# Kernel tuning notes

Measured on AMD Instinct MI355X. Metric: run time of the kernel, lower is better.

Reference implementation:

```python
import jax, jax.numpy as jnp
import numpy as np

B, N1, N2, C = 4, 1024, 128, 1152
H, D = 16, 72            # num_heads, head_dim (1152 = 16*72)
HID = 4608               # mlp hidden = 4*1152
ATTN_SCALE = D ** -0.5
RMS_SCALE = C ** 0.5     # quirk: RMSNorm built with dim=1152 though applied over d=72
LN_EPS = 1e-6


def setup_inputs() -> dict:
    key = jax.random.key(0)
    ks = iter(jax.random.split(key, 64))
    n = lambda shape, s=1.0: jax.random.normal(next(ks), shape, jnp.float32) * s
    W = 0.02  # weight init scale
    inp = {
        "x": n((B, N1, C)),
        "c": n((B, N2, C)),
        "global_c": n((B, C)),
        "ada_x_w": n((C, 6 * C), W), "ada_x_b": jnp.zeros((6 * C,)),
        "ada_c_w": n((C, 6 * C), W), "ada_c_b": jnp.zeros((6 * C,)),
        "g1x_g": jnp.ones((C,)), "g1x_b": jnp.zeros((C,)),
        "g2x_g": jnp.ones((C,)), "g2x_b": jnp.zeros((C,)),
        "g1c_g": jnp.ones((C,)), "g1c_b": jnp.zeros((C,)),
        "g2c_g": jnp.ones((C,)), "g2c_b": jnp.zeros((C,)),
        "qkv_x_w": n((C, 3 * C), W), "qkv_x_b": jnp.zeros((3 * C,)),
        "proj_x_w": n((C, C), W), "proj_x_b": jnp.zeros((C,)),
        "qkv_c_w": n((C, 3 * C), W), "qkv_c_b": jnp.zeros((3 * C,)),
        "proj_c_w": n((C, C), W), "proj_c_b": jnp.zeros((C,)),
        "gq_x": jnp.ones((1,)), "gk_x": jnp.ones((1,)),
        "gq_c": jnp.ones((1,)), "gk_c": jnp.ones((1,)),
        "mlp_x_w1": n((C, HID), W), "mlp_x_b1": jnp.zeros((HID,)),
        "mlp_x_w2": n((HID, C), W), "mlp_x_b2": jnp.zeros((C,)),
        "mlp_c_w1": n((C, HID), W), "mlp_c_b1": jnp.zeros((HID,)),
        "mlp_c_w2": n((HID, C), W), "mlp_c_b2": jnp.zeros((C,)),
    }
    return inp


def _ln(t, g, b):
    m = t.mean(-1, keepdims=True)
    v = ((t - m) ** 2).mean(-1, keepdims=True)
    return (t - m) * jax.lax.rsqrt(v + LN_EPS) * g + b


def _modulate(t, shift, scale):  # shift/scale: [B, C]
    return t * (1.0 + scale[:, None, :]) + shift[:, None, :]


def _rms(t, g):  # F.normalize over last dim, then * sqrt(1152) * g
    nrm = jnp.sqrt(jnp.sum(t * t, axis=-1, keepdims=True))
    return t / jnp.maximum(nrm, 1e-12) * (RMS_SCALE * g)


def _heads(t):  # [B, N, H*D] -> [B, H, N, D]
    Bq, Nq, _ = t.shape
    return t.reshape(Bq, Nq, H, D).transpose(0, 2, 1, 3)


def _mmdit_forward(x, c, global_c,
                   ada_x_w, ada_x_b, ada_c_w, ada_c_b,
                   g1x_g, g1x_b, g2x_g, g2x_b, g1c_g, g1c_b, g2c_g, g2c_b,
                   qkv_x_w, qkv_x_b, proj_x_w, proj_x_b,
                   qkv_c_w, qkv_c_b, proj_c_w, proj_c_b,
                   gq_x, gk_x, gq_c, gk_c,
                   mlp_x_w1, mlp_x_b1, mlp_x_w2, mlp_x_b2,
                   mlp_c_w1, mlp_c_b1, mlp_c_w2, mlp_c_b2):
    s = jax.nn.silu(global_c)
    mod_x = jnp.split(s @ ada_x_w + ada_x_b, 6, axis=-1)
    mod_c = jnp.split(s @ ada_c_w + ada_c_b, 6, axis=-1)
    (sh_msa_x, sc_msa_x, gt_msa_x, sh_mlp_x, sc_mlp_x, gt_mlp_x) = mod_x
    (sh_msa_c, sc_msa_c, gt_msa_c, sh_mlp_c, sc_mlp_c, gt_mlp_c) = mod_c

    xin = _modulate(_ln(x, g1x_g, g1x_b), sh_msa_x, sc_msa_x)
    cin = _modulate(_ln(c, g1c_g, g1c_b), sh_msa_c, sc_msa_c)

    qx, kx, vx = jnp.split(xin @ qkv_x_w + qkv_x_b, 3, axis=-1)
    qc, kc, vc = jnp.split(cin @ qkv_c_w + qkv_c_b, 3, axis=-1)
    qx, kx, vx = _heads(qx), _heads(kx), _heads(vx)
    qc, kc, vc = _heads(qc), _heads(kc), _heads(vc)
    qx, kx = _rms(qx, gq_x), _rms(kx, gk_x)
    qc, kc = _rms(qc, gq_c), _rms(kc, gk_c)

    q = jnp.concatenate([qx, qc], axis=2)  # [B,H,N1+N2,D]
    k = jnp.concatenate([kx, kc], axis=2)
    v = jnp.concatenate([vx, vc], axis=2)

    scores = jnp.einsum('bhnd,bhmd->bhnm', q, k) * ATTN_SCALE
    attn = jax.nn.softmax(scores, axis=-1)
    o = jnp.einsum('bhnm,bhmd->bhnd', attn, v)
    o = o.transpose(0, 2, 1, 3).reshape(B, N1 + N2, C)
    ox, oc = o[:, :N1], o[:, N1:]
    attn_x = ox @ proj_x_w + proj_x_b
    attn_c = oc @ proj_c_w + proj_c_b

    x = x + gt_msa_x[:, None, :] * attn_x
    c = c + gt_msa_c[:, None, :] * attn_c

    hx = _modulate(_ln(x, g2x_g, g2x_b), sh_mlp_x, sc_mlp_x)
    hx = jax.nn.gelu(hx @ mlp_x_w1 + mlp_x_b1, approximate=True) @ mlp_x_w2 + mlp_x_b2
    x = x + gt_mlp_x[:, None, :] * hx

    hc = _modulate(_ln(c, g2c_g, g2c_b), sh_mlp_c, sc_mlp_c)
    hc = jax.nn.gelu(hc @ mlp_c_w1 + mlp_c_b1, approximate=True) @ mlp_c_w2 + mlp_c_b2
    c = c + gt_mlp_c[:, None, :] * hc
    return x, c


def reference(x, c, global_c,
              ada_x_w, ada_x_b, ada_c_w, ada_c_b,
              g1x_g, g1x_b, g2x_g, g2x_b, g1c_g, g1c_b, g2c_g, g2c_b,
              qkv_x_w, qkv_x_b, proj_x_w, proj_x_b,
              qkv_c_w, qkv_c_b, proj_c_w, proj_c_b,
              gq_x, gk_x, gq_c, gk_c,
              mlp_x_w1, mlp_x_b1, mlp_x_w2, mlp_x_b2,
              mlp_c_w1, mlp_c_b1, mlp_c_w2, mlp_c_b2):
    return _mmdit_forward(x, c, global_c,
                          ada_x_w, ada_x_b, ada_c_w, ada_c_b,
                          g1x_g, g1x_b, g2x_g, g2x_b, g1c_g, g1c_b, g2c_g, g2c_b,
                          qkv_x_w, qkv_x_b, proj_x_w, proj_x_b,
                          qkv_c_w, qkv_c_b, proj_c_w, proj_c_b,
                          gq_x, gk_x, gq_c, gk_c,
                          mlp_x_w1, mlp_x_b1, mlp_x_w2, mlp_x_b2,
                          mlp_c_w1, mlp_c_b1, mlp_c_w2, mlp_c_b2)
```

## Files before the change

### kernel.cpp

```cpp
#include <hip/hip_runtime.h>

typedef unsigned short u16;
typedef unsigned int u32;
typedef __attribute__((ext_vector_type(8))) short bf16x8;
typedef __attribute__((ext_vector_type(4))) float f32x4;

#define MX_ 4096
#define NT_ 1152
#define C_  1152
#define DP_ 96
#define D_  72
#define H_  16
#define MT_ 4608

static __device__ __forceinline__ float b2f(u16 u){ union{u32 i; float f;} x; x.i=((u32)u)<<16; return x.f; }
static __device__ __forceinline__ u16 f2b(float f){ u32 i=__float_as_uint(f); return (u16)((i + 0x7FFFu + ((i>>16)&1u))>>16); }

static __device__ __forceinline__ void gl_lds16(const u16* g, u16* l){
  __builtin_amdgcn_global_load_lds((const __attribute__((address_space(1))) void*)g,
                                   (__attribute__((address_space(3))) void*)l, 16, 0, 0);
}

#define MFMA16(a,b,c) __builtin_amdgcn_mfma_f32_16x16x32_bf16(a,b,c,0,0,0)

struct TrArgs {
  const float* src[8]; u16* dst[8]; int K[8]; int N[8]; int start[9];
};

__global__ __launch_bounds__(256) void transpose_kernel(TrArgs a){
  int bx = blockIdx.x;
  int mi = 0;
  #pragma unroll
  for (int i = 0; i < 8; ++i) if (bx >= a.start[i+1]) mi = i+1;
  int t = bx - a.start[mi];
  int K = a.K[mi], N = a.N[mi];
  int ntk = K >> 5;
  int tk = t % ntk, tn = t / ntk;
  int k0 = tk*32, n0 = tn*32;
  __shared__ u16 lds[32][33];
  int c = threadIdx.x & 31, r = threadIdx.x >> 5;
  const float* src = a.src[mi];
  u16* dst = a.dst[mi];
  #pragma unroll
  for (int ii = 0; ii < 4; ++ii){
    int row = r + ii*8;
    lds[row][c] = f2b(src[(size_t)(k0+row)*N + n0 + c]);
  }
  __syncthreads();
  {
    int n = threadIdx.x >> 3, kg = threadIdx.x & 7;
    union { uint2 v; u16 e[4]; } o;
    #pragma unroll
    for (int j = 0; j < 4; ++j) o.e[j] = lds[kg*4 + j][n];
    *(uint2*)(dst + (size_t)(n0+n)*K + k0 + kg*4) = o.v;
  }
}

__global__ __launch_bounds__(256) void ada_kernel(const float* gc, const float* wx, const float* bx,
                                                  const float* wc, const float* bc,
                                                  float* mod_x, float* mod_c){
  __shared__ float s[4][C_];
  __shared__ float part[4][4][64];
  int tid = threadIdx.x;
  for (int i = tid; i < 4*C_; i += 256){
    float v = gc[i];
    s[i / C_][i % C_] = v / (1.f + __expf(-v));
  }
  __syncthreads();
  int jq = tid & 63;
  int kq = tid >> 6;
  int jg = blockIdx.x*64 + jq;
  int which = jg / 6912;
  int j = jg % 6912;
  const float* W = which ? wc : wx;
  float a0=0.f, a1=0.f, a2=0.f, a3=0.f;
  for (int k = kq*288; k < kq*288 + 288; ++k){
    float w = W[(size_t)k*6912 + j];
    a0 += s[0][k]*w; a1 += s[1][k]*w; a2 += s[2][k]*w; a3 += s[3][k]*w;
  }
  part[kq][0][jq]=a0; part[kq][1][jq]=a1; part[kq][2][jq]=a2; part[kq][3][jq]=a3;
  __syncthreads();
  if (kq == 0){
    float bb = (which ? bc : bx)[j];
    float* out = which ? mod_c : mod_x;
    #pragma unroll
    for (int b = 0; b < 4; ++b){
      out[(size_t)b*6912 + j] = part[0][b][jq] + part[1][b][jq] + part[2][b][jq] + part[3][b][jq] + bb;
    }
  }
}

__global__ __launch_bounds__(256) void ln_mod_kernel(
  const float* srcx, const float* srcc, const float* g, const float* bt,
  const float* gcn, const float* btc,
  const float* shx, const float* scx, const float* shc, const float* scc,
  u16* out)
{
  int m = blockIdx.x;
  bool isC = (m >= MX_);
  const float* src = isC ? srcc + (size_t)(m - MX_)*C_ : srcx + (size_t)m*C_;
  int bidx = isC ? ((m - MX_) >> 7) : (m >> 10);
  const float* gg = isC ? gcn : g;
  const float* bb = isC ? btc : bt;
  const float* sh = (isC ? shc : shx) + (size_t)bidx*6912;
  const float* sc = (isC ? scc : scx) + (size_t)bidx*6912;
  int tid = threadIdx.x;
  float lv[8];
  float sum = 0.f, sq = 0.f;
  if (tid < 144){
    float4 v0 = *(const float4*)(src + tid*8);
    float4 v1 = *(const float4*)(src + tid*8 + 4);
    lv[0]=v0.x; lv[1]=v0.y; lv[2]=v0.z; lv[3]=v0.w;
    lv[4]=v1.x; lv[5]=v1.y; lv[6]=v1.z; lv[7]=v1.w;
    #pragma unroll
    for (int j = 0; j < 8; ++j){ sum += lv[j]; sq += lv[j]*lv[j]; }
  }
  #pragma unroll
  for (int off = 1; off < 64; off <<= 1){ sum += __shfl_xor(sum, off); sq += __shfl_xor(sq, off); }
  __shared__ float rs[4], rq[4];
  int wave = tid >> 6, lane = tid & 63;
  if (lane == 0){ rs[wave] = sum; rq[wave] = sq; }
  __syncthreads();
  float S = rs[0]+rs[1]+rs[2]+rs[3];
  float Q = rq[0]+rq[1]+rq[2]+rq[3];
  float mean = S * (1.f/1152.f);
  float var  = Q * (1.f/1152.f) - mean*mean;
  float rstd = rsqrtf(var + 1e-6f);
  if (tid < 144){
    union { uint4 v; u16 s[8]; } o;
    #pragma unroll
    for (int j = 0; j < 8; ++j){
      int n = tid*8 + j;
      float val = (lv[j] - mean)*rstd*gg[n] + bb[n];
      val = val*(1.f + sc[n]) + sh[n];
      o.s[j] = f2b(val);
    }
    *(uint4*)(out + (size_t)m*C_ + tid*8) = o.v;
  }
}

__global__ __launch_bounds__(256) void reduce2_kernel(
  const float* p0, const float* p1,
  const float* residx, const float* residc,
  const float* modx, const float* modc,
  const float* biasx, const float* biasc,
  float* outx, float* outc)
{
  for (int i4 = blockIdx.x*256 + threadIdx.x; i4 < MT_*288; i4 += gridDim.x*256){
    int m = i4 / 288, n4 = (i4 % 288)*4;
    bool isC = (m >= MX_);
    int bidx = isC ? ((m - MX_) >> 7) : (m >> 10);
    const float* gate  = (isC ? modc : modx) + (size_t)bidx*6912;
    const float* bias  = isC ? biasc : biasx;
    const float* resid = isC ? residc + (size_t)(m - MX_)*C_ : residx + (size_t)m*C_;
    float* o = isC ? outc + (size_t)(m - MX_)*C_ : outx + (size_t)m*C_;
    float4 a = *(const float4*)(p0 + (size_t)m*C_ + n4);
    float4 b = *(const float4*)(p1 + (size_t)m*C_ + n4);
    float4 r = *(const float4*)(resid + n4);
    float4 ov;
    ov.x = r.x + gate[n4+0]*(a.x + b.x + bias[n4+0]);
    ov.y = r.y + gate[n4+1]*(a.y + b.y + bias[n4+1]);
    ov.z = r.z + gate[n4+2]*(a.z + b.z + bias[n4+2]);
    ov.w = r.w + gate[n4+3]*(a.w + b.w + bias[n4+3]);
    *(float4*)(o + n4) = ov;
  }
}

struct GemmArgs {
  const u16* A; int lda; int rowmap;
  const u16* BTx; const u16* BTc;
  const float* biasx; const float* biasc;
  void* outx; void* outc;
  const float* residx; const float* residc;
  const float* gatex; const float* gatec;
  int N, K, kLen;
};

static __device__ __forceinline__ int amap(int m, int rowmap){
  if (rowmap){
    if (m < MX_) return (m >> 10)*NT_ + (m & 1023);
    int mm = m - MX_;
    return (mm >> 7)*NT_ + 1024 + (mm & 127);
  }
  return m;
}

template<int EPI>
__global__ __launch_bounds__(256, 2) void gemm_kernel(GemmArgs g){
  __shared__ u16 As[128*64];
  __shared__ u16 Bs[128*64];
  int gx = gridDim.x, gy = gridDim.y;
  int nwg = gx*gy;
  int orig = blockIdx.y*gx + blockIdx.x;
  int q = nwg >> 3, r8 = nwg & 7;
  int xcd = orig & 7, wi = orig >> 3;
  int swz = (xcd < r8 ? xcd*(q+1) : r8*(q+1) + (xcd - r8)*q) + wi;
  int n0 = (swz % gx)*128, m0 = (swz / gx)*128;
  int kStart = blockIdx.z * g.kLen;
  bool isC = (m0 >= MX_);
  const u16* BT = isC ? g.BTc : g.BTx;
  int tid = threadIdx.x, wave = tid >> 6, lane = tid & 63;
  int lg = lane >> 4, lr = lane & 15;
  int wm = wave >> 1, wn = wave & 1;
  f32x4 acc[4][4] = {};

  const u16* Aaddr[4]; const u16* Baddr[4];
  #pragma unroll
  for (int i = 0; i < 4; ++i){
    int cb = (wave*4 + i)*64;
    int qq = cb + lane;
    int row = qq >> 3;
    int c16 = (qq & 7) ^ (row & 7);
    Aaddr[i] = g.A + (size_t)amap(m0 + row, g.rowmap)*g.lda + kStart + c16*8;
    Baddr[i] = BT + (size_t)(n0 + row)*g.K + kStart + c16*8;
  }
  for (int k0 = 0; k0 < g.kLen; k0 += 64){
    #pragma unroll
    for (int i = 0; i < 4; ++i){
      int cb = (wave*4 + i)*64;
      gl_lds16(Aaddr[i] + k0, As + cb*8);
      gl_lds16(Baddr[i] + k0, Bs + cb*8);
    }
    __syncthreads();
    #pragma unroll
    for (int kkI = 0; kkI < 2; ++kkI){
      bf16x8 af[4], bfr[4];
      #pragma unroll
      for (int mi = 0; mi < 4; ++mi){
        int row = wm*64 + mi*16 + lr;
        int c16 = (kkI*4 + lg) ^ (row & 7);
        af[mi] = *(const bf16x8*)&As[row*64 + c16*8];
      }
      #pragma unroll
      for (int ni = 0; ni < 4; ++ni){
        int row = wn*64 + ni*16 + lr;
        int c16 = (kkI*4 + lg) ^ (row & 7);
        bfr[ni] = *(const bf16x8*)&Bs[row*64 + c16*8];
      }
      #pragma unroll
      for (int mi = 0; mi < 4; ++mi)
        #pragma unroll
        for (int ni = 0; ni < 4; ++ni)
          acc[mi][ni] = MFMA16(af[mi], bfr[ni], acc[mi][ni]);
    }
    __syncthreads();
  }

  const float* bias  = isC ? g.biasc : g.biasx;
  const float* resid = isC ? g.residc : g.residx;
  void* out = isC ? g.outc : g.outx;
  const float* gate = nullptr;
  if (EPI == 2){
    int bidx = isC ? ((m0 - MX_) >> 7) : (m0 >> 10);
    gate = (isC ? g.gatec : g.gatex) + (size_t)bidx*6912;
  }
  int mbase = isC ? (m0 - MX_) : m0;
  float* pbase = nullptr;
  if (EPI == 3) pbase = blockIdx.z ? (float*)g.outc : (float*)g.outx;
  #pragma unroll
  for (int mi = 0; mi < 4; ++mi){
    #pragma unroll
    for (int r = 0; r < 4; ++r){
      #pragma unroll
      for (int ni = 0; ni < 4; ++ni){
        int n = n0 + wn*64 + ni*16 + lr;
        if (EPI == 3){
          size_t prow = (size_t)(m0 + wm*64 + mi*16 + lg*4 + r);
          pbase[prow*(size_t)g.N + n] = acc[mi][ni][r];
        } else {
          size_t orow = (size_t)(mbase + wm*64 + mi*16 + lg*4 + r);
          float v = acc[mi][ni][r] + bias[n];
          if (EPI == 1){
            float u = 0.7978845608028654f*(v + 0.044715f*v*v*v);
            v = 0.5f*v*(1.f + tanhf(u));
          }
          if (EPI == 2){
            v = resid[orow*(size_t)g.N + n] + gate[n]*v;
            ((float*)out)[orow*(size_t)g.N + n] = v;
          } else {
            ((u16*)out)[orow*(size_t)g.N + n] = f2b(v);
          }
        }
      }
    }
  }
}

__global__ __launch_bounds__(256) void rmshead_kernel(
  const u16* qkv, const float* gqx, const float* gkx, const float* gqc, const float* gkc,
  u16* qpad, u16* kpad, u16* vT)
{
  int tt = blockIdx.x, h = blockIdx.y, b = blockIdx.z;
  int t0 = tt*64;
  bool isC = (t0 >= 1024);
  size_t rowbase = isC ? (size_t)(MX_ + b*128 + (t0 - 1024)) : (size_t)(b*1024 + t0);
  __shared__ u16 sq[2][64][72];
  __shared__ u16 sv[64][72];
  __shared__ float nf[2][64];
  int tid = threadIdx.x;
  for (int s = tid; s < 1728; s += 256){
    int which = s / 576, rem = s % 576;
    int t = rem / 9, ch = rem % 9;
    uint4 v = *(const uint4*)(qkv + (rowbase + t)*3456 + which*C_ + h*D_ + ch*8);
    u16* dst = (which < 2) ? &sq[which][t][ch*8] : &sv[t][ch*8];
    *(uint4*)dst = v;
  }
  __syncthreads();
  {
    int row = tid >> 1, half = tid & 1;
    int which = row >> 6, t = row & 63;
    float ss = 0.f;
    for (int d = half*36; d < half*36 + 36; ++d){
      float v = b2f(sq[which][t][d]); ss += v*v;
    }
    ss += __shfl_xor(ss, 1);
    if (half == 0){
      const float* gp = (which == 0) ? (isC ? gqc : gqx) : (isC ? gkc : gkx);
      float f = 33.9411254970f * gp[0] / fmaxf(sqrtf(ss), 1e-12f);
      if (which == 0) f *= 0.17002324581205f;
      nf[which][t] = f;
    }
  }
  __syncthreads();
  size_t obase = ((size_t)(b*H_ + h)*NT_ + t0) * DP_;
  for (int s = tid; s < 1536; s += 256){
    int which = s / 768, rem = s % 768;
    int t = rem / 12, ch = rem % 12;
    float f = nf[which][t];
    union { uint4 v; u16 e[8]; } o;
    #pragma unroll
    for (int j = 0; j < 8; ++j){
      int d = ch*8 + j;
      o.e[j] = (d < D_) ? f2b(b2f(sq[which][t][d]) * f) : (u16)0;
    }
    *(uint4*)((which == 0 ? qpad : kpad) + obase + (size_t)t*DP_ + ch*8) = o.v;
  }
  size_t vbase = (size_t)(b*H_ + h)*80*NT_;
  for (int s = tid; s < 576; s += 256){
    int d = s / 8, ch = s % 8;
    union { uint4 v; u16 e[8]; } o;
    #pragma unroll
    for (int j = 0; j < 8; ++j) o.e[j] = sv[ch*8 + j][d];
    *(uint4*)(vT + vbase + (size_t)d*NT_ + t0 + ch*8) = o.v;
  }
  for (int s = tid; s < 512; s += 256){
    int d = 72 + (s >> 6), t = s & 63;
    vT[vbase + (size_t)d*NT_ + t0 + t] = (d == 72) ? (u16)0x3F80 : (u16)0;
  }
}

__global__ __launch_bounds__(256) __attribute__((amdgpu_waves_per_eu(1, 2))) void attn_kernel(
  const u16* qpad, const u16* kpad, const u16* vT, u16* O)
{
  __shared__ u16 Ps[4][32][40];
  int orig = blockIdx.x;
  int w = (orig & 7)*72 + (orig >> 3);
  int qtb = w % 9, hb = w / 9;
  int h = hb & 15, b = hb >> 4;
  int bh = b*H_ + h;
  int tid = threadIdx.x, wave = tid >> 6, lane = tid & 63;
  int lg = lane >> 4, lr = lane & 15;
  int q0 = qtb*128 + wave*32;

  const u16* qb = qpad + (size_t)bh*NT_*DP_;
  const u16* kb = kpad + (size_t)bh*NT_*DP_;
  const u16* vb = vT + (size_t)bh*80*NT_;

  bf16x8 qf[2][3];
  #pragma unroll
  for (int qt = 0; qt < 2; ++qt)
    #pragma unroll
    for (int kk = 0; kk < 3; ++kk)
      qf[qt][kk] = *(const bf16x8*)(qb + (size_t)(q0 + qt*16 + lr)*DP_ + kk*32 + lg*8);

  f32x4 acc[5][2] = {};
  float m0 = -1e30f, m1 = -1e30f;

  bf16x8 kfA[2][3], kfB[2][3], vf[5];
  auto LOADK = [&](bf16x8 (&kf)[2][3], int kvt){
    #pragma unroll
    for (int kt = 0; kt < 2; ++kt)
      #pragma unroll
      for (int kk = 0; kk < 3; ++kk)
        kf[kt][kk] = *(const bf16x8*)(kb + (size_t)(kvt*32 + kt*16 + lr)*DP_ + kk*32 + lg*8);
  };
  u16* prow0 = &Ps[wave][lr][0];
  u16* prow1 = &Ps[wave][16 + lr][0];

  auto TILE = [&](bf16x8 (&kf)[2][3], bf16x8 (&kfn)[2][3], int t){
    #pragma unroll
    for (int dc = 0; dc < 5; ++dc)
      vf[dc] = *(const bf16x8*)(vb + (size_t)(dc*16 + lr)*NT_ + t*32 + lg*8);
    if (t + 1 < 36) LOADK(kfn, t + 1);

    f32x4 st[2][2] = {};
    __builtin_amdgcn_s_setprio(1);
    #pragma unroll
    for (int kk = 0; kk < 3; ++kk){
      st[0][0] = MFMA16(kf[0][kk], qf[0][kk], st[0][0]);
      st[0][1] = MFMA16(kf[0][kk], qf[1][kk], st[0][1]);
      st[1][0] = MFMA16(kf[1][kk], qf[0][kk], st[1][0]);
      st[1][1] = MFMA16(kf[1][kk], qf[1][kk], st[1][1]);
    }
    __builtin_amdgcn_s_setprio(0);

    float pm0 = fmaxf(fmaxf(fmaxf(st[0][0][0], st[0][0][1]), fmaxf(st[0][0][2], st[0][0][3])),
                      fmaxf(fmaxf(st[1][0][0], st[1][0][1]), fmaxf(st[1][0][2], st[1][0][3])));
    float pm1 = fmaxf(fmaxf(fmaxf(st[0][1][0], st[0][1][1]), fmaxf(st[0][1][2], st[0][1][3])),
                      fmaxf(fmaxf(st[1][1][0], st[1][1][1]), fmaxf(st[1][1][2], st[1][1][3])));
    float tt = fmaxf(pm0 - m0, pm1 - m1);
    if (!__all(tt <= 11.5415603f)){
      float r0 = fmaxf(pm0, __shfl_xor(pm0, 16)); r0 = fmaxf(r0, __shfl_xor(r0, 32));
      float r1 = fmaxf(pm1, __shfl_xor(pm1, 16)); r1 = fmaxf(r1, __shfl_xor(r1, 32));
      float n0 = fmaxf(m0, r0), n1 = fmaxf(m1, r1);
      float f0 = exp2f(m0 - n0), f1 = exp2f(m1 - n1);
      m0 = n0; m1 = n1;
      #pragma unroll
      for (int dc = 0; dc < 5; ++dc)
        #pragma unroll
        for (int j = 0; j < 4; ++j){ acc[dc][0][j] *= f0; acc[dc][1][j] *= f1; }
    }
    #pragma unroll
    for (int kt = 0; kt < 2; ++kt){
      #pragma unroll
      for (int qt = 0; qt < 2; ++qt){
        float mm = qt ? m1 : m0;
        float e0 = exp2f(st[kt][qt][0] - mm);
        float e1 = exp2f(st[kt][qt][1] - mm);
        float e2 = exp2f(st[kt][qt][2] - mm);
        float e3 = exp2f(st[kt][qt][3] - mm);
        u32 lo, hi;
        asm("v_cvt_pk_bf16_f32 %0, %1, %2" : "=v"(lo) : "v"(e0), "v"(e1));
        asm("v_cvt_pk_bf16_f32 %0, %1, %2" : "=v"(hi) : "v"(e2), "v"(e3));
        uint2 pkd; pkd.x = lo; pkd.y = hi;
        *(uint2*)((qt ? prow1 : prow0) + kt*16 + lg*4) = pkd;
      }
    }
    asm volatile("s_waitcnt lgkmcnt(0)" ::: "memory");
    __builtin_amdgcn_sched_barrier(0);
    bf16x8 bp0 = *(const bf16x8*)(prow0 + lg*8);
    bf16x8 bp1 = *(const bf16x8*)(prow1 + lg*8);
    __builtin_amdgcn_s_setprio(1);
    #pragma unroll
    for (int dc = 0; dc < 5; ++dc){
      acc[dc][0] = MFMA16(vf[dc], bp0, acc[dc][0]);
      acc[dc][1] = MFMA16(vf[dc], bp1, acc[dc][1]);
    }
    __builtin_amdgcn_s_setprio(0);
  };

  LOADK(kfA, 0);
  for (int t2 = 0; t2 < 18; ++t2){
    TILE(kfA, kfB, 2*t2);
    TILE(kfB, kfA, 2*t2 + 1);
  }

  float l0 = __shfl(acc[4][0][0], 32 + lr);
  float l1 = __shfl(acc[4][1][0], 32 + lr);
  float rl0 = 1.f / l0, rl1 = 1.f / l1;
  #pragma unroll
  for (int dc = 0; dc < 5; ++dc){
    #pragma unroll
    for (int qt = 0; qt < 2; ++qt){
      if (dc < 4 || lg < 2){
        float rl = qt ? rl1 : rl0;
        union { uint2 v; u16 e[4]; } o;
        #pragma unroll
        for (int j = 0; j < 4; ++j) o.e[j] = f2b(acc[dc][qt][j] * rl);
        int tok = q0 + qt*16 + lr;
        *(uint2*)(O + ((size_t)b*NT_ + tok)*C_ + h*D_ + dc*16 + lg*4) = o.v;
      }
    }
  }
}

extern "C" void kernel_launch(void* const* d_in, const int* in_sizes, int n_in,
                              void* d_out, int out_size, void* d_ws, size_t ws_size,
                              hipStream_t stream)
{
  (void)in_sizes; (void)n_in; (void)out_size; (void)ws_size;
  const float* x        = (const float*)d_in[0];
  const float* c        = (const float*)d_in[1];
  const float* gc       = (const float*)d_in[2];
  const float* ada_x_w  = (const float*)d_in[3];
  const float* ada_x_b  = (const float*)d_in[4];
  const float* ada_c_w  = (const float*)d_in[5];
  const float* ada_c_b  = (const float*)d_in[6];
  const float* g1x_g    = (const float*)d_in[7];
  const float* g1x_b    = (const float*)d_in[8];
  const float* g2x_g    = (const float*)d_in[9];
  const float* g2x_b    = (const float*)d_in[10];
  const float* g1c_g    = (const float*)d_in[11];
  const float* g1c_b    = (const float*)d_in[12];
  const float* g2c_g    = (const float*)d_in[13];
  const float* g2c_b    = (const float*)d_in[14];
  const float* qkv_x_w  = (const float*)d_in[15];
  const float* qkv_x_b  = (const float*)d_in[16];
  const float* proj_x_w = (const float*)d_in[17];
  const float* proj_x_b = (const float*)d_in[18];
  const float* qkv_c_w  = (const float*)d_in[19];
  const float* qkv_c_b  = (const float*)d_in[20];
  const float* proj_c_w = (const float*)d_in[21];
  const float* proj_c_b = (const float*)d_in[22];
  const float* gq_x     = (const float*)d_in[23];
  const float* gk_x     = (const float*)d_in[24];
  const float* gq_c     = (const float*)d_in[25];
  const float* gk_c     = (const float*)d_in[26];
  const float* m_x_w1   = (const float*)d_in[27];
  const float* m_x_b1   = (const float*)d_in[28];
  const float* m_x_w2   = (const float*)d_in[29];
  const float* m_x_b2   = (const float*)d_in[30];
  const float* m_c_w1   = (const float*)d_in[31];
  const float* m_c_b1   = (const float*)d_in[32];
  const float* m_c_w2   = (const float*)d_in[33];
  const float* m_c_b2   = (const float*)d_in[34];
  float* out = (float*)d_out;

  char* ws = (char*)d_ws;
  size_t off = 0;
  auto alloc = [&](size_t bytes)->void*{ void* p = ws + off; off += (bytes + 255) & ~(size_t)255; return p; };
  u16* WTqx  = (u16*)alloc((size_t)3456*1152*2);
  u16* WTqc  = (u16*)alloc((size_t)3456*1152*2);
  u16* WTpx  = (u16*)alloc((size_t)1152*1152*2);
  u16* WTpc  = (u16*)alloc((size_t)1152*1152*2);
  u16* WTm1x = (u16*)alloc((size_t)4608*1152*2);
  u16* WTm2x = (u16*)alloc((size_t)1152*4608*2);
  u16* WTm1c = (u16*)alloc((size_t)4608*1152*2);
  u16* WTm2c = (u16*)alloc((size_t)1152*4608*2);
  float* mod_x = (float*)alloc((size_t)4*6912*4);
  float* mod_c = (float*)alloc((size_t)4*6912*4);
  u16* xin  = (u16*)alloc((size_t)4608*1152*2);
  u16* pool = (u16*)alloc((size_t)4608*4608*2);
  u16* qpad = (u16*)alloc((size_t)64*1152*96*2 + 4096);
  u16* kpad = (u16*)alloc((size_t)64*1152*96*2 + 4096);
  u16* vTb  = (u16*)alloc((size_t)64*80*1152*2 + 4096);
  u16* Obuf = (u16*)alloc((size_t)4*1152*1152*2);
  float* x1c1 = (float*)alloc((size_t)4608*1152*4);
  float* fc2p0 = (float*)qpad;
  float* fc2p1 = fc2p0 + (size_t)MT_*C_;
  float* projp0 = (float*)qpad;

  {
    TrArgs ta;
    const float* srcs[8] = {qkv_x_w, qkv_c_w, proj_x_w, proj_c_w, m_x_w1, m_x_w2, m_c_w1, m_c_w2};
    u16* dsts[8]         = {WTqx, WTqc, WTpx, WTpc, WTm1x, WTm2x, WTm1c, WTm2c};
    int Ks[8] = {1152,1152,1152,1152,1152,4608,1152,4608};
    int Ns[8] = {3456,3456,1152,1152,4608,1152,4608,1152};
    int st = 0;
    for (int i = 0; i < 8; ++i){
      ta.src[i] = srcs[i]; ta.dst[i] = dsts[i]; ta.K[i] = Ks[i]; ta.N[i] = Ns[i];
      ta.start[i] = st; st += (Ks[i]/32)*(Ns[i]/32);
    }
    ta.start[8] = st;
    transpose_kernel<<<dim3(st), dim3(256), 0, stream>>>(ta);
  }
  ada_kernel<<<dim3(216), dim3(256), 0, stream>>>(gc, ada_x_w, ada_x_b, ada_c_w, ada_c_b, mod_x, mod_c);
  ln_mod_kernel<<<dim3(4608), dim3(256), 0, stream>>>(
      x, c, g1x_g, g1x_b, g1c_g, g1c_b,
      mod_x + 0, mod_x + 1152, mod_c + 0, mod_c + 1152, xin);
  {
    GemmArgs ga{};
    ga.A = xin; ga.lda = 1152; ga.rowmap = 0;
    ga.BTx = WTqx; ga.BTc = WTqc; ga.biasx = qkv_x_b; ga.biasc = qkv_c_b;
    ga.outx = pool; ga.outc = pool + (size_t)4096*3456;
    ga.N = 3456; ga.K = 1152; ga.kLen = 1152;
    gemm_kernel<0><<<dim3(27,36), dim3(256), 0, stream>>>(ga);
  }
  rmshead_kernel<<<dim3(18,16,4), dim3(256), 0, stream>>>(pool, gq_x, gk_x, gq_c, gk_c, qpad, kpad, vTb);
  attn_kernel<<<dim3(576), dim3(256), 0, stream>>>(qpad, kpad, vTb, Obuf);
  {
    GemmArgs ga{};
    ga.A = Obuf; ga.lda = 1152; ga.rowmap = 1;
    ga.BTx = WTpx; ga.BTc = WTpc;
    ga.outx = projp0; ga.outc = x1c1;
    ga.N = 1152; ga.K = 1152; ga.kLen = 576;
    gemm_kernel<3><<<dim3(9,36,2), dim3(256), 0, stream>>>(ga);
  }
  reduce2_kernel<<<dim3(2048), dim3(256), 0, stream>>>(
      projp0, x1c1, x, c,
      mod_x + 2*1152, mod_c + 2*1152, proj_x_b, proj_c_b,
      x1c1, x1c1 + (size_t)4096*1152);
  ln_mod_kernel<<<dim3(4608), dim3(256), 0, stream>>>(
      x1c1, x1c1 + (size_t)4096*1152, g2x_g, g2x_b, g2c_g, g2c_b,
      mod_x + 3*1152, mod_x + 4*1152, mod_c + 3*1152, mod_c + 4*1152, xin);
  {
    GemmArgs ga{};
    ga.A = xin; ga.lda = 1152; ga.rowmap = 0;
    ga.BTx = WTm1x; ga.BTc = WTm1c; ga.biasx = m_x_b1; ga.biasc = m_c_b1;
    ga.outx = pool; ga.outc = pool + (size_t)4096*4608;
    ga.N = 4608; ga.K = 1152; ga.kLen = 1152;
    gemm_kernel<1><<<dim3(36,36), dim3(256), 0, stream>>>(ga);
  }
  {
    GemmArgs ga{};
    ga.A = pool; ga.lda = 4608; ga.rowmap = 0;
    ga.BTx = WTm2x; ga.BTc = WTm2c;
    ga.outx = fc2p0; ga.outc = fc2p1;
    ga.N = 1152; ga.K = 4608; ga.kLen = 2304;
    gemm_kernel<3><<<dim3(9,36,2), dim3(256), 0, stream>>>(ga);
  }
  reduce2_kernel<<<dim3(2048), dim3(256), 0, stream>>>(
      fc2p0, fc2p1, x1c1, x1c1 + (size_t)4096*1152,
      mod_x + 5*1152, mod_c + 5*1152, m_x_b2, m_c_b2,
      out, out + (size_t)4096*1152);
}
```

Measured before the change: 445.9 us.

## Split attention KV range in two with separate combine kernel

Attention now runs each query tile over half of the key/value range, doubling the grid from 576 to 1152 blocks. Partial bf16 accumulators, row sums and running maxima go to scratch in the pool buffer. A new combine kernel merges the two halves with log-sum-exp weights. The aim is better CU occupancy and load balance on the 256-CU part. The cost is an extra launch, extra global traffic, and accumulators rounded to bf16 before the merge.

```diff
diff --git a/kernel.cpp b/kernel.cpp
--- a/kernel.cpp
+++ b/kernel.cpp
@@ -12,6 +12,7 @@
 #define D_  72
 #define H_  16
 #define MT_ 4608
+#define RWS_ 73728
 
 static __device__ __forceinline__ float b2f(u16 u){ union{u32 i; float f;} x; x.i=((u32)u)<<16; return x.f; }
 static __device__ __forceinline__ u16 f2b(float f){ u32 i=__float_as_uint(f); return (u16)((i + 0x7FFFu + ((i>>16)&1u))>>16); }
@@ -166,6 +167,30 @@
   }
 }
 
+__global__ __launch_bounds__(256) void attncomb_kernel(
+  const u16* accP, const float* lP, const float* mP, u16* O)
+{
+  for (int i = blockIdx.x*256 + threadIdx.x; i < RWS_*18; i += gridDim.x*256){
+    int row = i / 18, cg = i % 18;
+    float m1 = mP[row], m2 = mP[RWS_ + row];
+    float mm = fmaxf(m1, m2);
+    float w1 = exp2f(m1 - mm), w2 = exp2f(m2 - mm);
+    float rL = 1.f / (lP[row]*w1 + lP[RWS_ + row]*w2);
+    const u16* a1 = accP + (size_t)row*80 + cg*4;
+    const u16* a2 = accP + ((size_t)RWS_ + row)*80 + cg*4;
+    union { uint2 v; u16 e[4]; } o;
+    #pragma unroll
+    for (int j = 0; j < 4; ++j)
+      o.e[j] = f2b((b2f(a1[j])*w1 + b2f(a2[j])*w2) * rL);
+    int b = row >> 14;
+    int h = (row >> 10) & 15;
+    int bh = row / NT_;
+    int tok = row - bh*NT_;
+    b = bh >> 4; h = bh & 15;
+    *(uint2*)(O + ((size_t)b*NT_ + tok)*C_ + h*D_ + cg*4) = o.v;
+  }
+}
+
 struct GemmArgs {
   const u16* A; int lda; int rowmap;
   const u16* BTx; const u16* BTc;
@@ -350,17 +375,20 @@
 }
 
 __global__ __launch_bounds__(256) __attribute__((amdgpu_waves_per_eu(1, 2))) void attn_kernel(
-  const u16* qpad, const u16* kpad, const u16* vT, u16* O)
+  const u16* qpad, const u16* kpad, const u16* vT,
+  u16* accP, float* lP, float* mP)
 {
   __shared__ u16 Ps[4][32][40];
   int orig = blockIdx.x;
-  int w = (orig & 7)*72 + (orig >> 3);
-  int qtb = w % 9, hb = w / 9;
+  int w = (orig & 7)*144 + (orig >> 3);
+  int sub = w % 18, hb = w / 18;
+  int qtb = sub >> 1, half = sub & 1;
   int h = hb & 15, b = hb >> 4;
   int bh = b*H_ + h;
   int tid = threadIdx.x, wave = tid >> 6, lane = tid & 63;
   int lg = lane >> 4, lr = lane & 15;
   int q0 = qtb*128 + wave*32;
+  int tbase = half*18;
 
   const u16* qb = qpad + (size_t)bh*NT_*DP_;
   const u16* kb = kpad + (size_t)bh*NT_*DP_;
@@ -391,7 +419,7 @@
     #pragma unroll
     for (int dc = 0; dc < 5; ++dc)
       vf[dc] = *(const bf16x8*)(vb + (size_t)(dc*16 + lr)*NT_ + t*32 + lg*8);
-    if (t + 1 < 36) LOADK(kfn, t + 1);
+    if (t + 1 < tbase + 18) LOADK(kfn, t + 1);
 
     f32x4 st[2][2] = {};
     __builtin_amdgcn_s_setprio(1);
@@ -449,28 +477,25 @@
     __builtin_amdgcn_s_setprio(0);
   };
 
-  LOADK(kfA, 0);
-  for (int t2 = 0; t2 < 18; ++t2){
-    TILE(kfA, kfB, 2*t2);
-    TILE(kfB, kfA, 2*t2 + 1);
-  }
-
-  float l0 = __shfl(acc[4][0][0], 32 + lr);
-  float l1 = __shfl(acc[4][1][0], 32 + lr);
-  float rl0 = 1.f / l0, rl1 = 1.f / l1;
+  LOADK(kfA, tbase);
+  for (int t2 = 0; t2 < 9; ++t2){
+    TILE(kfA, kfB, tbase + 2*t2);
+    TILE(kfB, kfA, tbase + 2*t2 + 1);
+  }
+
   #pragma unroll
-  for (int dc = 0; dc < 5; ++dc){
-    #pragma unroll
-    for (int qt = 0; qt < 2; ++qt){
-      if (dc < 4 || lg < 2){
-        float rl = qt ? rl1 : rl0;
-        union { uint2 v; u16 e[4]; } o;
-        #pragma unroll
-        for (int j = 0; j < 4; ++j) o.e[j] = f2b(acc[dc][qt][j] * rl);
-        int tok = q0 + qt*16 + lr;
-        *(uint2*)(O + ((size_t)b*NT_ + tok)*C_ + h*D_ + dc*16 + lg*4) = o.v;
-      }
-    }
+  for (int qt = 0; qt < 2; ++qt){
+    size_t row = (size_t)half*RWS_ + (size_t)bh*NT_ + (q0 + qt*16 + lr);
+    u16* arow = accP + row*80;
+    #pragma unroll
+    for (int dc = 0; dc < 5; ++dc){
+      union { uint2 v; u16 e[4]; } o;
+      #pragma unroll
+      for (int j = 0; j < 4; ++j) o.e[j] = f2b(acc[dc][qt][j]);
+      *(uint2*)(arow + dc*16 + lg*4) = o.v;
+    }
+    if (lg == 2) lP[row] = acc[4][qt][0];
+    if (lg == 0) mP[row] = qt ? m1 : m0;
   }
 }
 
@@ -536,6 +561,9 @@
   u16* vTb  = (u16*)alloc((size_t)64*80*1152*2 + 4096);
   u16* Obuf = (u16*)alloc((size_t)4*1152*1152*2);
   float* x1c1 = (float*)alloc((size_t)4608*1152*4);
+  u16* accP = pool;
+  float* lP = (float*)(pool + (size_t)2*RWS_*80);
+  float* mP = lP + (size_t)2*RWS_;
   float* fc2p0 = (float*)qpad;
   float* fc2p1 = fc2p0 + (size_t)MT_*C_;
   float* projp0 = (float*)qpad;
@@ -567,7 +595,8 @@
     gemm_kernel<0><<<dim3(27,36), dim3(256), 0, stream>>>(ga);
   }
   rmshead_kernel<<<dim3(18,16,4), dim3(256), 0, stream>>>(pool, gq_x, gk_x, gq_c, gk_c, qpad, kpad, vTb);
-  attn_kernel<<<dim3(576), dim3(256), 0, stream>>>(qpad, kpad, vTb, Obuf);
+  attn_kernel<<<dim3(1152), dim3(256), 0, stream>>>(qpad, kpad, vTb, accP, lP, mP);
+  attncomb_kernel<<<dim3(2048), dim3(256), 0, stream>>>(accP, lP, mP, Obuf);
   {
     GemmArgs ga{};
     ga.A = Obuf; ga.lda = 1152; ga.rowmap = 1;
```

After: 445.3 us. Within noise of the previous version (-0.1%).

## Split KV range across two wave groups in attention and merge via LDS

Applied to the files above, without the earlier changes.

Doubles the attention block to 512 threads. Two groups of four waves each process half of the key/value tiles for the same query rows. The second group writes its partial accumulators and running maxima to shared memory, and the first group rescales and combines them before normalizing and storing. This is meant to raise the number of active waves on the GPU at the cost of extra LDS traffic, a block barrier, and tighter per-thread register budgets.

```diff
diff --git a/kernel.cpp b/kernel.cpp
--- a/kernel.cpp
+++ b/kernel.cpp
@@ -349,10 +349,11 @@
   }
 }
 
-__global__ __launch_bounds__(256) __attribute__((amdgpu_waves_per_eu(1, 2))) void attn_kernel(
+__global__ __launch_bounds__(512) void attn_kernel(
   const u16* qpad, const u16* kpad, const u16* vT, u16* O)
 {
-  __shared__ u16 Ps[4][32][40];
+  __shared__ u16 Ps[8][32][40];
+  __shared__ float comb[4][64][43];
   int orig = blockIdx.x;
   int w = (orig & 7)*72 + (orig >> 3);
   int qtb = w % 9, hb = w / 9;
@@ -360,7 +361,8 @@
   int bh = b*H_ + h;
   int tid = threadIdx.x, wave = tid >> 6, lane = tid & 63;
   int lg = lane >> 4, lr = lane & 15;
-  int q0 = qtb*128 + wave*32;
+  int q0 = qtb*128 + (wave & 3)*32;
+  int tbase = (wave >> 2)*18;
 
   const u16* qb = qpad + (size_t)bh*NT_*DP_;
   const u16* kb = kpad + (size_t)bh*NT_*DP_;
@@ -391,7 +393,7 @@
     #pragma unroll
     for (int dc = 0; dc < 5; ++dc)
       vf[dc] = *(const bf16x8*)(vb + (size_t)(dc*16 + lr)*NT_ + t*32 + lg*8);
-    if (t + 1 < 36) LOADK(kfn, t + 1);
+    if (t + 1 < tbase + 18) LOADK(kfn, t + 1);
 
     f32x4 st[2][2] = {};
     __builtin_amdgcn_s_setprio(1);
@@ -449,26 +451,50 @@
     __builtin_amdgcn_s_setprio(0);
   };
 
-  LOADK(kfA, 0);
-  for (int t2 = 0; t2 < 18; ++t2){
-    TILE(kfA, kfB, 2*t2);
-    TILE(kfB, kfA, 2*t2 + 1);
-  }
-
-  float l0 = __shfl(acc[4][0][0], 32 + lr);
-  float l1 = __shfl(acc[4][1][0], 32 + lr);
-  float rl0 = 1.f / l0, rl1 = 1.f / l1;
-  #pragma unroll
-  for (int dc = 0; dc < 5; ++dc){
-    #pragma unroll
-    for (int qt = 0; qt < 2; ++qt){
-      if (dc < 4 || lg < 2){
-        float rl = qt ? rl1 : rl0;
-        union { uint2 v; u16 e[4]; } o;
+  LOADK(kfA, tbase);
+  for (int t2 = 0; t2 < 9; ++t2){
+    TILE(kfA, kfB, tbase + 2*t2);
+    TILE(kfB, kfA, tbase + 2*t2 + 1);
+  }
+
+  if (wave >= 4){
+    float* cb = &comb[wave - 4][lane][0];
+    #pragma unroll
+    for (int dc = 0; dc < 5; ++dc)
+      #pragma unroll
+      for (int qt = 0; qt < 2; ++qt)
         #pragma unroll
-        for (int j = 0; j < 4; ++j) o.e[j] = f2b(acc[dc][qt][j] * rl);
-        int tok = q0 + qt*16 + lr;
-        *(uint2*)(O + ((size_t)b*NT_ + tok)*C_ + h*D_ + dc*16 + lg*4) = o.v;
+        for (int j = 0; j < 4; ++j) cb[dc*8 + qt*4 + j] = acc[dc][qt][j];
+    cb[40] = m0; cb[41] = m1;
+  }
+  __syncthreads();
+  if (wave < 4){
+    const float* cb = &comb[wave][lane][0];
+    float mb0 = cb[40], mb1 = cb[41];
+    float M0 = fmaxf(m0, mb0), M1 = fmaxf(m1, mb1);
+    float wa0 = exp2f(m0 - M0), wb0 = exp2f(mb0 - M0);
+    float wa1 = exp2f(m1 - M1), wb1 = exp2f(mb1 - M1);
+    float cl0 = acc[4][0][0]*wa0 + cb[4*8 + 0*4 + 0]*wb0;
+    float cl1 = acc[4][1][0]*wa1 + cb[4*8 + 1*4 + 0]*wb1;
+    float l0 = __shfl(cl0, 32 + lr);
+    float l1 = __shfl(cl1, 32 + lr);
+    float rl0 = 1.f / l0, rl1 = 1.f / l1;
+    #pragma unroll
+    for (int dc = 0; dc < 5; ++dc){
+      #pragma unroll
+      for (int qt = 0; qt < 2; ++qt){
+        if (dc < 4 || lg < 2){
+          float wa = qt ? wa1 : wa0, wb = qt ? wb1 : wb0;
+          float rl = qt ? rl1 : rl0;
+          union { uint2 v; u16 e[4]; } o;
+          #pragma unroll
+          for (int j = 0; j < 4; ++j){
+            float cv = acc[dc][qt][j]*wa + cb[dc*8 + qt*4 + j]*wb;
+            o.e[j] = f2b(cv * rl);
+          }
+          int tok = q0 + qt*16 + lr;
+          *(uint2*)(O + ((size_t)b*NT_ + tok)*C_ + h*D_ + dc*16 + lg*4) = o.v;
+        }
       }
     }
   }
@@ -567,7 +593,7 @@
     gemm_kernel<0><<<dim3(27,36), dim3(256), 0, stream>>>(ga);
   }
   rmshead_kernel<<<dim3(18,16,4), dim3(256), 0, stream>>>(pool, gq_x, gk_x, gq_c, gk_c, qpad, kpad, vTb);
-  attn_kernel<<<dim3(576), dim3(256), 0, stream>>>(qpad, kpad, vTb, Obuf);
+  attn_kernel<<<dim3(576), dim3(512), 0, stream>>>(qpad, kpad, vTb, Obuf);
   {
     GemmArgs ga{};
     ga.A = Obuf; ga.lda = 1152; ga.rowmap = 1;
```

Result: no change. 451.5 us (+1.3%).
